# Optimization experiments

Hardware: AMD Instinct MI355X
Metric: run time of the kernel (lower is better)

The kernel has to match this reference:

```python
import jax, jax.numpy as jnp
import numpy as np

N = 100000   # nodes
E = 3200000  # edges (avg degree 32)
F_IN = 32    # node_feature_dim
H = 64       # hidden_dim
L = 4        # num_layers
A = 6158     # action_space_size
G = 64       # graphs in batch


def setup_inputs() -> dict:
    key = jax.random.key(0)
    ks = jax.random.split(key, 12)
    x = jax.random.normal(ks[0], (N, F_IN), dtype=jnp.float32)
    edge_index = jax.random.randint(ks[1], (2, E), 0, N, dtype=jnp.int64)
    batch = jnp.sort(jax.random.randint(ks[2], (N,), 0, G, dtype=jnp.int64))
    s_in = 1.0 / np.sqrt(F_IN)
    s_h = 1.0 / np.sqrt(H)
    W_enc = jax.random.normal(ks[3], (H, F_IN), dtype=jnp.float32) * s_in
    b_enc = jax.random.normal(ks[4], (H,), dtype=jnp.float32) * s_in
    Wl = jax.random.normal(ks[5], (L, H, H), dtype=jnp.float32) * s_h  # SAGEConv lin_l (aggregated)
    bl = jax.random.normal(ks[6], (L, H), dtype=jnp.float32) * s_h
    Wr = jax.random.normal(ks[7], (L, H, H), dtype=jnp.float32) * s_h  # SAGEConv lin_r (root, no bias)
    Wp = jax.random.normal(ks[8], (A, H), dtype=jnp.float32) * s_h
    bp = jax.random.normal(ks[9], (A,), dtype=jnp.float32) * s_h
    Wv = jax.random.normal(ks[10], (1, H), dtype=jnp.float32) * s_h
    bv = jax.random.normal(ks[11], (1,), dtype=jnp.float32) * s_h
    return {"x": x, "edge_index": edge_index, "batch": batch,
            "W_enc": W_enc, "b_enc": b_enc, "Wl": Wl, "bl": bl, "Wr": Wr,
            "Wp": Wp, "bp": bp, "Wv": Wv, "bv": bv}


def reference(x, edge_index, batch, W_enc, b_enc, Wl, bl, Wr, Wp, bp, Wv, bv):
    src, dst = edge_index[0], edge_index[1]
    # in-degree for mean aggregation (isolated nodes -> 0 aggregate, clamp deg to 1)
    deg = jax.ops.segment_sum(jnp.ones((E,), x.dtype), dst, num_segments=N)
    inv_deg = (1.0 / jnp.maximum(deg, 1.0))[:, None]  # [N,1]

    h = jax.nn.relu(x @ W_enc.T + b_enc)  # [N,H]
    for i in range(L):
        agg = jax.ops.segment_sum(h[src], dst, num_segments=N) * inv_deg  # mean of neighbors
        conv = agg @ Wl[i].T + bl[i] + h @ Wr[i].T  # SAGEConv
        h = jax.nn.relu(conv) + h  # residual

    # global_mean_pool over batch segment ids
    counts = jax.ops.segment_sum(jnp.ones((N,), h.dtype), batch, num_segments=G)
    graph_repr = jax.ops.segment_sum(h, batch, num_segments=G) / jnp.maximum(counts, 1.0)[:, None]  # [G,H]

    policy = graph_repr @ Wp.T + bp            # [G,A]
    value = jnp.tanh(graph_repr @ Wv.T + bv)   # [G,1]
    return policy, value.squeeze(-1)
```

## Files before the change

kernel.cpp:

```cpp
#include <hip/hip_runtime.h>
#include <hip/hip_bf16.h>

#define N_NODES 100000
#define N_EDGES 3200000
#define F_IN    32
#define H       64
#define L_LAYERS 4
#define A_SZ    6158
#define G_SZ    64

#define NBUCK 391
#define EPB   8192
#define NEBLK 391

typedef __attribute__((ext_vector_type(8))) short bf16x8;
typedef __attribute__((ext_vector_type(4))) float f32x4;

__device__ __forceinline__ float bflo(unsigned u) { return __uint_as_float(u << 16); }
__device__ __forceinline__ float bfhi(unsigned u) { return __uint_as_float(u & 0xffff0000u); }
__device__ __forceinline__ float bfu(unsigned short u) { return __uint_as_float(((unsigned)u) << 16); }
__device__ __forceinline__ unsigned short f2bf(float f) {
    union { __hip_bfloat16 b; unsigned short u; } c;
    c.b = __float2bfloat16(f);
    return c.u;
}
__device__ __forceinline__ bf16x8 ldfrag(const unsigned short* p) {
    union { uint4 u; bf16x8 v; } c;
    c.u = *(const uint4*)p;
    return c.v;
}
__device__ __forceinline__ bf16x8 cvt8(const float* p) {
    float4 lo = *(const float4*)p;
    float4 hi = *(const float4*)(p + 4);
    bf16x8 r;
    r[0] = (short)f2bf(lo.x); r[1] = (short)f2bf(lo.y);
    r[2] = (short)f2bf(lo.z); r[3] = (short)f2bf(lo.w);
    r[4] = (short)f2bf(hi.x); r[5] = (short)f2bf(hi.y);
    r[6] = (short)f2bf(hi.z); r[7] = (short)f2bf(hi.w);
    return r;
}


__global__ __launch_bounds__(256) void bucket_hist_kernel(const int* __restrict__ ei,
                                                          int* __restrict__ bhist) {
    __shared__ int hist[NBUCK];
    int t = threadIdx.x;
    for (int i = t; i < NBUCK; i += 256) hist[i] = 0;
    __syncthreads();
    int base = blockIdx.x * EPB;
    #pragma unroll
    for (int i = 0; i < EPB / 256; ++i) {
        int e = base + i * 256 + t;
        if (e < N_EDGES) atomicAdd(&hist[ei[N_EDGES + e] >> 8], 1);
    }
    __syncthreads();
    for (int i = t; i < NBUCK; i += 256)
        if (hist[i]) atomicAdd(&bhist[i], hist[i]);
}

__global__ void bucket_scan_kernel(const int* __restrict__ bhist,
                                   int* __restrict__ bucket_base,
                                   int* __restrict__ bcursor) {
    __shared__ int s[512];
    int t = threadIdx.x;
    int v = (t < NBUCK) ? bhist[t] : 0;
    s[t] = v;
    __syncthreads();
    for (int off = 1; off < 512; off <<= 1) {
        int x = (t >= off) ? s[t - off] : 0;
        __syncthreads();
        s[t] += x;
        __syncthreads();
    }
    if (t < NBUCK) {
        int excl = s[t] - v;
        bucket_base[t] = excl;
        bcursor[t] = excl;
    }
    if (t == 0) bucket_base[NBUCK] = N_EDGES;
}

__global__ __launch_bounds__(256) void bucket_scatter_kernel(const int* __restrict__ ei,
                                                             int* __restrict__ bcursor,
                                                             unsigned int* __restrict__ pairs) {
    __shared__ int hist[NBUCK];
    __shared__ int cur[NBUCK];
    int t = threadIdx.x;
    for (int i = t; i < NBUCK; i += 256) hist[i] = 0;
    __syncthreads();
    int base = blockIdx.x * EPB;
    #pragma unroll
    for (int i = 0; i < EPB / 256; ++i) {
        int e = base + i * 256 + t;
        if (e < N_EDGES) atomicAdd(&hist[ei[N_EDGES + e] >> 8], 1);
    }
    __syncthreads();
    for (int i = t; i < NBUCK; i += 256) {
        int c = hist[i];
        cur[i] = c ? atomicAdd(&bcursor[i], c) : 0;
    }
    __syncthreads();
    #pragma unroll
    for (int i = 0; i < EPB / 256; ++i) {
        int e = base + i * 256 + t;
        if (e < N_EDGES) {
            int src = ei[e];
            int dst = ei[N_EDGES + e];
            int b = dst >> 8;
            int idx = atomicAdd(&cur[b], 1);
            pairs[idx] = ((unsigned int)(dst & 255) << 17) | (unsigned int)src;
        }
    }
}

__global__ __launch_bounds__(256) void bucket_rank_kernel(const unsigned int* __restrict__ pairs,
                                                          const int* __restrict__ bucket_base,
                                                          int* __restrict__ row_start,
                                                          float* __restrict__ inv_deg,
                                                          int* __restrict__ src_sorted) {
    __shared__ int cnt[256];
    __shared__ int scn[256];
    __shared__ int cur[256];
    int b = blockIdx.x;
    int t = threadIdx.x;
    int nb0 = b << 8;
    int e0 = bucket_base[b];
    int e1 = bucket_base[b + 1];
    cnt[t] = 0;
    __syncthreads();
    for (int e = e0 + t; e < e1; e += 256)
        atomicAdd(&cnt[pairs[e] >> 17], 1);
    __syncthreads();
    int v = cnt[t];
    scn[t] = v;
    __syncthreads();
    for (int off = 1; off < 256; off <<= 1) {
        int x = (t >= off) ? scn[t - off] : 0;
        __syncthreads();
        scn[t] += x;
        __syncthreads();
    }
    int excl = scn[t] - v;
    int n = nb0 + t;
    if (n < N_NODES) {
        row_start[n] = e0 + excl;
        inv_deg[n] = 1.0f / (float)max(v, 1);
    }
    cur[t] = e0 + excl;
    __syncthreads();
    for (int e = e0 + t; e < e1; e += 256) {
        unsigned int p = pairs[e];
        int slot = atomicAdd(&cur[p >> 17], 1);
        src_sorted[slot] = (int)(p & 0x1FFFFu);
    }
    if (b == 0 && t == 0) row_start[N_NODES] = N_EDGES;
}


__global__ __launch_bounds__(256) void encoder_kernel(const float* __restrict__ x,
                                                      const float* __restrict__ W_enc,
                                                      const float* __restrict__ b_enc,
                                                      unsigned short* __restrict__ h16) {
    __shared__ float Wt[F_IN][H + 1];
    __shared__ float xl[4][F_IN];
    int t = threadIdx.x;
    #pragma unroll
    for (int r = 0; r < 8; ++r) {
        int idx = r * 256 + t;
        Wt[idx & 31][idx >> 5] = W_enc[idx];
    }
    int nb = blockIdx.x * 4;
    if (t < 128) ((float*)xl)[t] = x[nb * F_IN + t];
    __syncthreads();
    int n = t >> 6;
    int f = t & 63;
    float acc = b_enc[f];
    #pragma unroll
    for (int k = 0; k < F_IN; ++k) acc += xl[n][k] * Wt[k][f];
    h16[(size_t)(nb + n) * H + f] = f2bf(fmaxf(acc, 0.0f));
}


__global__ __launch_bounds__(256) void aggregate_kernel(const unsigned short* __restrict__ h16,
                                                        const int* __restrict__ row_start,
                                                        const int* __restrict__ src_sorted,
                                                        const float* __restrict__ inv_deg,
                                                        unsigned int* __restrict__ agg16) {
    int t = threadIdx.x;
    int wave = (blockIdx.x << 2) + (t >> 6);
    int lane = t & 63;
    int half = lane >> 5;
    int j = lane & 31;
    int node = (wave << 1) + half;
    if (node >= N_NODES) return;
    int s = row_start[node];
    int e = row_start[node + 1];
    float a0 = 0.f, a1 = 0.f, b0 = 0.f, b1 = 0.f;
    float c0 = 0.f, c1 = 0.f, d0 = 0.f, d1 = 0.f;
    int i = s;
    for (; i + 3 < e; i += 4) {
        int s0 = src_sorted[i], s1 = src_sorted[i + 1];
        int s2 = src_sorted[i + 2], s3 = src_sorted[i + 3];
        unsigned u0 = *(const unsigned*)(h16 + (size_t)s0 * H + 2 * j);
        unsigned u1 = *(const unsigned*)(h16 + (size_t)s1 * H + 2 * j);
        unsigned u2 = *(const unsigned*)(h16 + (size_t)s2 * H + 2 * j);
        unsigned u3 = *(const unsigned*)(h16 + (size_t)s3 * H + 2 * j);
        a0 += bflo(u0); a1 += bfhi(u0);
        b0 += bflo(u1); b1 += bfhi(u1);
        c0 += bflo(u2); c1 += bfhi(u2);
        d0 += bflo(u3); d1 += bfhi(u3);
    }
    for (; i < e; ++i) {
        unsigned u = *(const unsigned*)(h16 + (size_t)src_sorted[i] * H + 2 * j);
        a0 += bflo(u); a1 += bfhi(u);
    }
    float inv = inv_deg[node];
    float r0 = ((a0 + b0) + (c0 + d0)) * inv;
    float r1 = ((a1 + b1) + (c1 + d1)) * inv;
    agg16[(size_t)node * 32 + j] = (unsigned)f2bf(r0) | ((unsigned)f2bf(r1) << 16);
}


__global__ __launch_bounds__(256) void update_kernel(const float* __restrict__ Wl,
                                                     const float* __restrict__ bl,
                                                     const float* __restrict__ Wr,
                                                     const unsigned short* __restrict__ agg16,
                                                     unsigned short* __restrict__ h16) {
    int t = threadIdx.x;
    int w = t >> 6;
    int lane = t & 63;
    int r16 = lane & 15;
    int kc = lane >> 4;
    int nb = blockIdx.x * 16;
    int f0 = w * 16;

    const unsigned short* aRow = agg16 + (size_t)(nb + r16) * H;
    const unsigned short* hRow = h16 + (size_t)(nb + r16) * H;
    bf16x8 aA0 = ldfrag(aRow + kc * 8);
    bf16x8 aA1 = ldfrag(aRow + 32 + kc * 8);
    bf16x8 hA0 = ldfrag(hRow + kc * 8);
    bf16x8 hA1 = ldfrag(hRow + 32 + kc * 8);

    const float* wlRow = Wl + (size_t)(f0 + r16) * H;
    const float* wrRow = Wr + (size_t)(f0 + r16) * H;
    bf16x8 bL0 = cvt8(wlRow + kc * 8);
    bf16x8 bL1 = cvt8(wlRow + 32 + kc * 8);
    bf16x8 bR0 = cvt8(wrRow + kc * 8);
    bf16x8 bR1 = cvt8(wrRow + 32 + kc * 8);

    float bias = bl[f0 + r16];
    float hres[4];
    #pragma unroll
    for (int j = 0; j < 4; ++j)
        hres[j] = bfu(h16[(size_t)(nb + kc * 4 + j) * H + f0 + r16]);

    __syncthreads();

    f32x4 acc = {0.f, 0.f, 0.f, 0.f};
    acc = __builtin_amdgcn_mfma_f32_16x16x32_bf16(aA0, bL0, acc, 0, 0, 0);
    acc = __builtin_amdgcn_mfma_f32_16x16x32_bf16(aA1, bL1, acc, 0, 0, 0);
    acc = __builtin_amdgcn_mfma_f32_16x16x32_bf16(hA0, bR0, acc, 0, 0, 0);
    acc = __builtin_amdgcn_mfma_f32_16x16x32_bf16(hA1, bR1, acc, 0, 0, 0);

    #pragma unroll
    for (int j = 0; j < 4; ++j) {
        float v = fmaxf(acc[j] + bias, 0.f) + hres[j];
        h16[(size_t)(nb + kc * 4 + j) * H + f0 + r16] = f2bf(v);
    }
}


__global__ __launch_bounds__(256) void pool_kernel(const unsigned short* __restrict__ h16,
                                                   const int* __restrict__ batch,
                                                   float* __restrict__ gsum,
                                                   float* __restrict__ gcount) {
    int w = blockIdx.x * 4 + (threadIdx.x >> 6);
    int f = threadIdx.x & 63;
    int n0 = w * 32;
    if (n0 >= N_NODES) return;
    int n1 = min(n0 + 32, N_NODES);
    int g0 = batch[n0];
    int gend = batch[n1 - 1];
    if (g0 == gend) {
        float a0 = 0.f, a1 = 0.f, a2 = 0.f, a3 = 0.f;
        int n = n0;
        for (; n + 3 < n1; n += 4) {
            a0 += bfu(h16[(size_t)n * H + f]);
            a1 += bfu(h16[(size_t)(n + 1) * H + f]);
            a2 += bfu(h16[(size_t)(n + 2) * H + f]);
            a3 += bfu(h16[(size_t)(n + 3) * H + f]);
        }
        for (; n < n1; ++n) a0 += bfu(h16[(size_t)n * H + f]);
        atomicAdd(&gsum[g0 * H + f], (a0 + a1) + (a2 + a3));
        if (f == 0) atomicAdd(&gcount[g0], (float)(n1 - n0));
    } else {
        int curg = g0;
        float acc = 0.f;
        int cnt = 0;
        for (int n = n0; n < n1; ++n) {
            int g = batch[n];
            if (g != curg) {
                atomicAdd(&gsum[curg * H + f], acc);
                if (f == 0) atomicAdd(&gcount[curg], (float)cnt);
                acc = 0.f; cnt = 0; curg = g;
            }
            acc += bfu(h16[(size_t)n * H + f]);
            ++cnt;
        }
        atomicAdd(&gsum[curg * H + f], acc);
        if (f == 0) atomicAdd(&gcount[curg], (float)cnt);
    }
}


__global__ __launch_bounds__(256) void policy_kernel(const float* __restrict__ gsum,
                                                     const float* __restrict__ gcount,
                                                     const float* __restrict__ Wp,
                                                     const float* __restrict__ bp,
                                                     float* __restrict__ out) {
    __shared__ float gr[H];
    int g = blockIdx.y;
    int t = threadIdx.x;
    if (t < H) {
        float inv = 1.0f / fmaxf(gcount[g], 1.0f);
        gr[t] = gsum[g * H + t] * inv;
    }
    __syncthreads();
    int a = blockIdx.x * 256 + t;
    if (a >= A_SZ) return;
    const float4* wp4 = (const float4*)(Wp + a * H);
    float acc = bp[a];
    #pragma unroll
    for (int c = 0; c < 16; ++c) {
        float4 wv = wp4[c];
        acc += gr[4 * c + 0] * wv.x + gr[4 * c + 1] * wv.y
             + gr[4 * c + 2] * wv.z + gr[4 * c + 3] * wv.w;
    }
    out[g * A_SZ + a] = acc;
}

__global__ void value_kernel(const float* __restrict__ gsum, const float* __restrict__ gcount,
                             const float* __restrict__ Wv, const float* __restrict__ bv,
                             float* __restrict__ out) {
    int g = threadIdx.x;
    if (g >= G_SZ) return;
    float inv = 1.0f / fmaxf(gcount[g], 1.0f);
    float acc = bv[0];
    #pragma unroll
    for (int k = 0; k < H; ++k) acc += gsum[g * H + k] * inv * Wv[k];
    out[G_SZ * A_SZ + g] = tanhf(acc);
}


extern "C" void kernel_launch(void* const* d_in, const int* in_sizes, int n_in,
                              void* d_out, int out_size, void* d_ws, size_t ws_size,
                              hipStream_t stream) {
    const float* x     = (const float*)d_in[0];
    const int*   ei    = (const int*)d_in[1];
    const int*   batch = (const int*)d_in[2];
    const float* W_enc = (const float*)d_in[3];
    const float* b_enc = (const float*)d_in[4];
    const float* Wl    = (const float*)d_in[5];
    const float* bl    = (const float*)d_in[6];
    const float* Wr    = (const float*)d_in[7];
    const float* Wp    = (const float*)d_in[8];
    const float* bp    = (const float*)d_in[9];
    const float* Wv    = (const float*)d_in[10];
    const float* bv    = (const float*)d_in[11];
    float* out = (float*)d_out;

    char* ws = (char*)d_ws;
    size_t off = 0;
    auto alloc = [&](size_t bytes) {
        char* p = ws + off;
        off = (off + bytes + 255) & ~(size_t)255;
        return p;
    };
    unsigned short* h16   = (unsigned short*)alloc((size_t)N_NODES * H * 2);
    unsigned int*   agg16 = (unsigned int*)alloc((size_t)N_NODES * H * 2);
    int* row_start        = (int*)alloc((size_t)(N_NODES + 1) * 4);
    float* inv_deg        = (float*)alloc((size_t)N_NODES * 4);
    int* src_sorted       = (int*)alloc((size_t)N_EDGES * 4);
    unsigned int* pairs   = (unsigned int*)alloc((size_t)N_EDGES * 4);
    int* bhist            = (int*)alloc((NBUCK + 8) * 4);
    int* bucket_base      = (int*)alloc((NBUCK + 8) * 4);
    int* bcursor          = (int*)alloc((NBUCK + 8) * 4);
    float* gsum           = (float*)alloc((size_t)(G_SZ * H + G_SZ) * 4);
    float* gcount         = gsum + G_SZ * H;

    hipMemsetAsync(bhist, 0, NBUCK * 4, stream);
    bucket_hist_kernel<<<NEBLK, 256, 0, stream>>>(ei, bhist);
    bucket_scan_kernel<<<1, 512, 0, stream>>>(bhist, bucket_base, bcursor);
    bucket_scatter_kernel<<<NEBLK, 256, 0, stream>>>(ei, bcursor, pairs);
    bucket_rank_kernel<<<NBUCK, 256, 0, stream>>>(pairs, bucket_base, row_start,
                                                  inv_deg, src_sorted);

    encoder_kernel<<<N_NODES / 4, 256, 0, stream>>>(x, W_enc, b_enc, h16);

    const int UPD_BLOCKS = N_NODES / 16;
    for (int l = 0; l < L_LAYERS; ++l) {
        aggregate_kernel<<<N_NODES / 8, 256, 0, stream>>>(h16, row_start, src_sorted,
                                                          inv_deg, agg16);
        update_kernel<<<UPD_BLOCKS, 256, 0, stream>>>(Wl + (size_t)l * H * H, bl + l * H,
                                                      Wr + (size_t)l * H * H,
                                                      (const unsigned short*)agg16, h16);
    }

    hipMemsetAsync(gsum, 0, (size_t)(G_SZ * H + G_SZ) * 4, stream);
    const int POOL_BLOCKS = (N_NODES / 32 + 3) / 4 + 1;
    pool_kernel<<<POOL_BLOCKS, 256, 0, stream>>>(h16, batch, gsum, gcount);
    policy_kernel<<<dim3((A_SZ + 255) / 256, G_SZ), 256, 0, stream>>>(gsum, gcount, Wp, bp, out);
    value_kernel<<<1, 64, 0, stream>>>(gsum, gcount, Wv, bv, out);
}
```

Baseline: 668.5 us.

## Use buffer loads with pre-scaled offsets in gather, prepack bf16 weights, batch policy GEMV

The edge source indices are stored pre-multiplied by the row byte stride, so the aggregation gather can use raw buffer loads with 32-bit offsets, and the gather loop is unrolled to 8 edges for more loads in flight. Layer weights are converted to bf16 once in a new small kernel instead of per block in the update kernel. The policy head now computes 8 graphs per block, so each Wp row is read once per 8 graphs. This adds a kernel launch and a compile-time fallback path for when the buffer builtins are unavailable.

Result: faster. 604.6 us (-9.6%).

```diff
diff --git a/kernel.cpp b/kernel.cpp
--- a/kernel.cpp
+++ b/kernel.cpp
@@ -29,16 +29,12 @@
     c.u = *(const uint4*)p;
     return c.v;
 }
-__device__ __forceinline__ bf16x8 cvt8(const float* p) {
-    float4 lo = *(const float4*)p;
-    float4 hi = *(const float4*)(p + 4);
-    bf16x8 r;
-    r[0] = (short)f2bf(lo.x); r[1] = (short)f2bf(lo.y);
-    r[2] = (short)f2bf(lo.z); r[3] = (short)f2bf(lo.w);
-    r[4] = (short)f2bf(hi.x); r[5] = (short)f2bf(hi.y);
-    r[6] = (short)f2bf(hi.z); r[7] = (short)f2bf(hi.w);
-    return r;
-}
+
+#if __has_builtin(__builtin_amdgcn_make_buffer_rsrc) && __has_builtin(__builtin_amdgcn_raw_buffer_load_b32)
+#define USE_BUFFER_LOAD 1
+#else
+#define USE_BUFFER_LOAD 0
+#endif
 
 
 __global__ __launch_bounds__(256) void bucket_hist_kernel(const int* __restrict__ ei,
@@ -151,9 +147,19 @@
     for (int e = e0 + t; e < e1; e += 256) {
         unsigned int p = pairs[e];
         int slot = atomicAdd(&cur[p >> 17], 1);
-        src_sorted[slot] = (int)(p & 0x1FFFFu);
+        src_sorted[slot] = (int)((p & 0x1FFFFu) << 7);
     }
     if (b == 0 && t == 0) row_start[N_NODES] = N_EDGES;
+}
+
+
+__global__ __launch_bounds__(256) void wconv_kernel(const float* __restrict__ Wl,
+                                                    const float* __restrict__ Wr,
+                                                    unsigned short* __restrict__ wl16,
+                                                    unsigned short* __restrict__ wr16) {
+    int i = blockIdx.x * 256 + threadIdx.x;
+    wl16[i] = f2bf(Wl[i]);
+    wr16[i] = f2bf(Wr[i]);
 }
 
 
@@ -195,25 +201,43 @@
     if (node >= N_NODES) return;
     int s = row_start[node];
     int e = row_start[node + 1];
+    int off = 4 * j;
+
+#if USE_BUFFER_LOAD
+    __amdgpu_buffer_rsrc_t rs = __builtin_amdgcn_make_buffer_rsrc(
+        (void*)h16, (short)0, (int)((size_t)N_NODES * 128), 0x00020000);
+    #define GATHER(vo) __builtin_amdgcn_raw_buffer_load_b32(rs, (vo) + off, 0, 0)
+#else
+    const char* hb = (const char*)h16;
+    #define GATHER(vo) (*(const unsigned*)(hb + (size_t)(unsigned)((vo) + off)))
+#endif
+
     float a0 = 0.f, a1 = 0.f, b0 = 0.f, b1 = 0.f;
     float c0 = 0.f, c1 = 0.f, d0 = 0.f, d1 = 0.f;
     int i = s;
-    for (; i + 3 < e; i += 4) {
-        int s0 = src_sorted[i], s1 = src_sorted[i + 1];
+    for (; i + 7 < e; i += 8) {
+        int s0 = src_sorted[i],     s1 = src_sorted[i + 1];
         int s2 = src_sorted[i + 2], s3 = src_sorted[i + 3];
-        unsigned u0 = *(const unsigned*)(h16 + (size_t)s0 * H + 2 * j);
-        unsigned u1 = *(const unsigned*)(h16 + (size_t)s1 * H + 2 * j);
-        unsigned u2 = *(const unsigned*)(h16 + (size_t)s2 * H + 2 * j);
-        unsigned u3 = *(const unsigned*)(h16 + (size_t)s3 * H + 2 * j);
+        int s4 = src_sorted[i + 4], s5 = src_sorted[i + 5];
+        int s6 = src_sorted[i + 6], s7 = src_sorted[i + 7];
+        unsigned u0 = GATHER(s0), u1 = GATHER(s1);
+        unsigned u2 = GATHER(s2), u3 = GATHER(s3);
+        unsigned u4 = GATHER(s4), u5 = GATHER(s5);
+        unsigned u6 = GATHER(s6), u7 = GATHER(s7);
         a0 += bflo(u0); a1 += bfhi(u0);
         b0 += bflo(u1); b1 += bfhi(u1);
         c0 += bflo(u2); c1 += bfhi(u2);
         d0 += bflo(u3); d1 += bfhi(u3);
+        a0 += bflo(u4); a1 += bfhi(u4);
+        b0 += bflo(u5); b1 += bfhi(u5);
+        c0 += bflo(u6); c1 += bfhi(u6);
+        d0 += bflo(u7); d1 += bfhi(u7);
     }
     for (; i < e; ++i) {
-        unsigned u = *(const unsigned*)(h16 + (size_t)src_sorted[i] * H + 2 * j);
+        unsigned u = GATHER(src_sorted[i]);
         a0 += bflo(u); a1 += bfhi(u);
     }
+    #undef GATHER
     float inv = inv_deg[node];
     float r0 = ((a0 + b0) + (c0 + d0)) * inv;
     float r1 = ((a1 + b1) + (c1 + d1)) * inv;
@@ -221,9 +245,9 @@
 }
 
 
-__global__ __launch_bounds__(256) void update_kernel(const float* __restrict__ Wl,
+__global__ __launch_bounds__(256) void update_kernel(const unsigned short* __restrict__ wl16,
                                                      const float* __restrict__ bl,
-                                                     const float* __restrict__ Wr,
+                                                     const unsigned short* __restrict__ wr16,
                                                      const unsigned short* __restrict__ agg16,
                                                      unsigned short* __restrict__ h16) {
     int t = threadIdx.x;
@@ -241,18 +265,18 @@
     bf16x8 hA0 = ldfrag(hRow + kc * 8);
     bf16x8 hA1 = ldfrag(hRow + 32 + kc * 8);
 
-    const float* wlRow = Wl + (size_t)(f0 + r16) * H;
-    const float* wrRow = Wr + (size_t)(f0 + r16) * H;
-    bf16x8 bL0 = cvt8(wlRow + kc * 8);
-    bf16x8 bL1 = cvt8(wlRow + 32 + kc * 8);
-    bf16x8 bR0 = cvt8(wrRow + kc * 8);
-    bf16x8 bR1 = cvt8(wrRow + 32 + kc * 8);
+    const unsigned short* wlRow = wl16 + (size_t)(f0 + r16) * H;
+    const unsigned short* wrRow = wr16 + (size_t)(f0 + r16) * H;
+    bf16x8 bL0 = ldfrag(wlRow + kc * 8);
+    bf16x8 bL1 = ldfrag(wlRow + 32 + kc * 8);
+    bf16x8 bR0 = ldfrag(wrRow + kc * 8);
+    bf16x8 bR1 = ldfrag(wrRow + 32 + kc * 8);
 
     float bias = bl[f0 + r16];
     float hres[4];
     #pragma unroll
-    for (int j = 0; j < 4; ++j)
-        hres[j] = bfu(h16[(size_t)(nb + kc * 4 + j) * H + f0 + r16]);
+    for (int jq = 0; jq < 4; ++jq)
+        hres[jq] = bfu(h16[(size_t)(nb + kc * 4 + jq) * H + f0 + r16]);
 
     __syncthreads();
 
@@ -263,9 +287,9 @@
     acc = __builtin_amdgcn_mfma_f32_16x16x32_bf16(hA1, bR1, acc, 0, 0, 0);
 
     #pragma unroll
-    for (int j = 0; j < 4; ++j) {
-        float v = fmaxf(acc[j] + bias, 0.f) + hres[j];
-        h16[(size_t)(nb + kc * 4 + j) * H + f0 + r16] = f2bf(v);
+    for (int jq = 0; jq < 4; ++jq) {
+        float v = fmaxf(acc[jq] + bias, 0.f) + hres[jq];
+        h16[(size_t)(nb + kc * 4 + jq) * H + f0 + r16] = f2bf(v);
     }
 }
 
@@ -318,25 +342,36 @@
                                                      const float* __restrict__ Wp,
                                                      const float* __restrict__ bp,
                                                      float* __restrict__ out) {
-    __shared__ float gr[H];
-    int g = blockIdx.y;
-    int t = threadIdx.x;
-    if (t < H) {
-        float inv = 1.0f / fmaxf(gcount[g], 1.0f);
-        gr[t] = gsum[g * H + t] * inv;
+    __shared__ float gr[8][H];
+    int g0 = blockIdx.y * 8;
+    int t = threadIdx.x;
+    #pragma unroll
+    for (int r = 0; r < 2; ++r) {
+        int idx = r * 256 + t;
+        int gg = idx >> 6, f = idx & 63;
+        float inv = 1.0f / fmaxf(gcount[g0 + gg], 1.0f);
+        gr[gg][f] = gsum[(g0 + gg) * H + f] * inv;
     }
     __syncthreads();
     int a = blockIdx.x * 256 + t;
     if (a >= A_SZ) return;
     const float4* wp4 = (const float4*)(Wp + a * H);
-    float acc = bp[a];
+    float bpa = bp[a];
+    float acc[8];
+    #pragma unroll
+    for (int gg = 0; gg < 8; ++gg) acc[gg] = bpa;
     #pragma unroll
     for (int c = 0; c < 16; ++c) {
         float4 wv = wp4[c];
-        acc += gr[4 * c + 0] * wv.x + gr[4 * c + 1] * wv.y
-             + gr[4 * c + 2] * wv.z + gr[4 * c + 3] * wv.w;
-    }
-    out[g * A_SZ + a] = acc;
+        #pragma unroll
+        for (int gg = 0; gg < 8; ++gg) {
+            acc[gg] += gr[gg][4 * c + 0] * wv.x + gr[gg][4 * c + 1] * wv.y
+                     + gr[gg][4 * c + 2] * wv.z + gr[gg][4 * c + 3] * wv.w;
+        }
+    }
+    #pragma unroll
+    for (int gg = 0; gg < 8; ++gg)
+        out[(g0 + gg) * A_SZ + a] = acc[gg];
 }
 
 __global__ void value_kernel(const float* __restrict__ gsum, const float* __restrict__ gcount,
@@ -385,6 +420,8 @@
     int* bhist            = (int*)alloc((NBUCK + 8) * 4);
     int* bucket_base      = (int*)alloc((NBUCK + 8) * 4);
     int* bcursor          = (int*)alloc((NBUCK + 8) * 4);
+    unsigned short* wl16  = (unsigned short*)alloc((size_t)L_LAYERS * H * H * 2);
+    unsigned short* wr16  = (unsigned short*)alloc((size_t)L_LAYERS * H * H * 2);
     float* gsum           = (float*)alloc((size_t)(G_SZ * H + G_SZ) * 4);
     float* gcount         = gsum + G_SZ * H;
 
@@ -395,20 +432,21 @@
     bucket_rank_kernel<<<NBUCK, 256, 0, stream>>>(pairs, bucket_base, row_start,
                                                   inv_deg, src_sorted);
 
+    wconv_kernel<<<(L_LAYERS * H * H) / 256, 256, 0, stream>>>(Wl, Wr, wl16, wr16);
     encoder_kernel<<<N_NODES / 4, 256, 0, stream>>>(x, W_enc, b_enc, h16);
 
     const int UPD_BLOCKS = N_NODES / 16;
     for (int l = 0; l < L_LAYERS; ++l) {
         aggregate_kernel<<<N_NODES / 8, 256, 0, stream>>>(h16, row_start, src_sorted,
                                                           inv_deg, agg16);
-        update_kernel<<<UPD_BLOCKS, 256, 0, stream>>>(Wl + (size_t)l * H * H, bl + l * H,
-                                                      Wr + (size_t)l * H * H,
+        update_kernel<<<UPD_BLOCKS, 256, 0, stream>>>(wl16 + (size_t)l * H * H, bl + l * H,
+                                                      wr16 + (size_t)l * H * H,
                                                       (const unsigned short*)agg16, h16);
     }
 
     hipMemsetAsync(gsum, 0, (size_t)(G_SZ * H + G_SZ) * 4, stream);
     const int POOL_BLOCKS = (N_NODES / 32 + 3) / 4 + 1;
     pool_kernel<<<POOL_BLOCKS, 256, 0, stream>>>(h16, batch, gsum, gcount);
-    policy_kernel<<<dim3((A_SZ + 255) / 256, G_SZ), 256, 0, stream>>>(gsum, gcount, Wp, bp, out);
+    policy_kernel<<<dim3((A_SZ + 255) / 256, 8), 256, 0, stream>>>(gsum, gcount, Wp, bp, out);
     value_kernel<<<1, 64, 0, stream>>>(gsum, gcount, Wv, bv, out);
 }
```
